# Kernel tuning notes

Hardware: AMD Instinct MI355X
Metric: run time of the kernel (lower is better)

The kernel has to match this reference:

```python
import jax, jax.numpy as jnp
import numpy as np

TAU = 0.1  # temperature (registered buffer, non-trainable)
EPS = 1e-12  # F.normalize eps


def setup_inputs() -> dict:
    key = jax.random.key(0)
    k1, k2 = jax.random.split(key)
    B, C = 4096, 512
    z1 = jax.random.normal(k1, (B, C), dtype=jnp.float32)
    z2 = jax.random.normal(k2, (B, C), dtype=jnp.float32)
    return {"z1": z1, "z2": z2}


def _l2_normalize(x):
    # matches F.normalize(p=2, dim=1): x / max(||x||, eps)
    n = jnp.sqrt(jnp.sum(x * x, axis=1, keepdims=True))
    return x / jnp.maximum(n, EPS)


def reference(z1, z2):
    B = z1.shape[0]
    N = 2 * B
    z = jnp.concatenate([_l2_normalize(z1), _l2_normalize(z2)], axis=0)  # [2B, C]
    # cosine similarity of unit vectors == dot product -> single GEMM
    S = jnp.exp((z @ z.T) / TAU)  # [2B, 2B]
    rows = jnp.arange(N)
    pos_cols = (rows + B) % N  # mask[r, c]=1 iff r == (c+B) mod 2B  <=> c == (r+B) mod 2B
    positive = S[rows, pos_cols]                 # [2B]
    # negatives = row sum over ~mask; note the original INCLUDES the diagonal
    negative = jnp.sum(S, axis=1) - positive     # [2B]
    pairs_loss = -jnp.log(positive / negative)   # [2B]
    loss = pairs_loss.reshape(2, B).sum(axis=0) / N  # [B]
    return loss.mean()  # reduce=True
```

## Files before the change

kernel.cpp:

```cpp
#include <hip/hip_runtime.h>
#include <hip/hip_bf16.h>


#define BDIM 4096
#define CDIM 512
#define NROWS 8192

typedef __attribute__((ext_vector_type(4))) float f32x4;
typedef __attribute__((ext_vector_type(8))) short bf16x8;

__device__ __forceinline__ unsigned short f2bf_rne(float x) {
    unsigned u = __float_as_uint(x);
    u += 0x7fffu + ((u >> 16) & 1u);
    return (unsigned short)(u >> 16);
}

__global__ __launch_bounds__(256) void normalize_kernel(
    const float* __restrict__ z1, const float* __restrict__ z2,
    unsigned short* __restrict__ zb, float* __restrict__ pos10) {
    const int w = threadIdx.x >> 6, lane = threadIdx.x & 63;
    const int r = blockIdx.x * 4 + w;
    const float4* p1 = (const float4*)(z1 + (size_t)r * CDIM);
    const float4* p2 = (const float4*)(z2 + (size_t)r * CDIM);
    float4 a0 = p1[lane], a1 = p1[64 + lane];
    float4 b0 = p2[lane], b1 = p2[64 + lane];
    float s1 = a0.x * a0.x + a0.y * a0.y + a0.z * a0.z + a0.w * a0.w +
               a1.x * a1.x + a1.y * a1.y + a1.z * a1.z + a1.w * a1.w;
    float s2 = b0.x * b0.x + b0.y * b0.y + b0.z * b0.z + b0.w * b0.w +
               b1.x * b1.x + b1.y * b1.y + b1.z * b1.z + b1.w * b1.w;
    float d = a0.x * b0.x + a0.y * b0.y + a0.z * b0.z + a0.w * b0.w +
              a1.x * b1.x + a1.y * b1.y + a1.z * b1.z + a1.w * b1.w;
#pragma unroll
    for (int m = 1; m < 64; m <<= 1) {
        s1 += __shfl_xor(s1, m, 64);
        s2 += __shfl_xor(s2, m, 64);
        d += __shfl_xor(d, m, 64);
    }
    const float n1 = fmaxf(sqrtf(s1), 1e-12f);
    const float n2 = fmaxf(sqrtf(s2), 1e-12f);
    const float i1 = 1.0f / n1, i2 = 1.0f / n2;
    ushort4 o;
    ushort4* q1 = (ushort4*)(zb + (size_t)r * CDIM);
    ushort4* q2 = (ushort4*)(zb + (size_t)(r + BDIM) * CDIM);
    o.x = f2bf_rne(a0.x * i1); o.y = f2bf_rne(a0.y * i1);
    o.z = f2bf_rne(a0.z * i1); o.w = f2bf_rne(a0.w * i1);
    q1[lane] = o;
    o.x = f2bf_rne(a1.x * i1); o.y = f2bf_rne(a1.y * i1);
    o.z = f2bf_rne(a1.z * i1); o.w = f2bf_rne(a1.w * i1);
    q1[64 + lane] = o;
    o.x = f2bf_rne(b0.x * i2); o.y = f2bf_rne(b0.y * i2);
    o.z = f2bf_rne(b0.z * i2); o.w = f2bf_rne(b0.w * i2);
    q2[lane] = o;
    o.x = f2bf_rne(b1.x * i2); o.y = f2bf_rne(b1.y * i2);
    o.z = f2bf_rne(b1.z * i2); o.w = f2bf_rne(b1.w * i2);
    q2[64 + lane] = o;
    if (lane == 0) pos10[r] = (d / (n1 * n2)) * 10.0f;
}

__global__ __launch_bounds__(256) void simgemm_kernel(
    const unsigned short* __restrict__ Z, float* __restrict__ rowsum) {
    const int bx = blockIdx.x, by = blockIdx.y;
    if (bx < by) return;
    const bool diag = (bx == by);

    __shared__ unsigned short Alds[128 * 64];
    __shared__ unsigned short Blds[128 * 64];

    const int t = threadIdx.x;
    const int lane = t & 63, w = t >> 6;
    const int wr = w >> 1, wc = w & 1;

    f32x4 acc[4][4] = {};

    const int srow = t >> 3;
    const int scolb = (((t & 7) ^ ((t >> 3) & 7)) << 4);
    const char* Zb = (const char*)Z;

    for (int k0 = 0; k0 < CDIM; k0 += 64) {
#pragma unroll
        for (int i = 0; i < 4; ++i) {
            const char* ga = Zb + ((size_t)(by * 128 + i * 32 + srow) << 10) + (k0 << 1) + scolb;
            __builtin_amdgcn_global_load_lds(
                (const __attribute__((address_space(1))) void*)ga,
                (__attribute__((address_space(3))) void*)(Alds + i * 2048 + w * 512),
                16, 0, 0);
        }
#pragma unroll
        for (int i = 0; i < 4; ++i) {
            const char* gb = Zb + ((size_t)(bx * 128 + i * 32 + srow) << 10) + (k0 << 1) + scolb;
            __builtin_amdgcn_global_load_lds(
                (const __attribute__((address_space(1))) void*)gb,
                (__attribute__((address_space(3))) void*)(Blds + i * 2048 + w * 512),
                16, 0, 0);
        }
        __syncthreads();

        const int sw = (lane & 7) << 4;
#pragma unroll
        for (int kk = 0; kk < 2; ++kk) {
            const int koff = (((lane >> 4) << 4) + kk * 64) ^ sw;
            bf16x8 af[4], bfr[4];
#pragma unroll
            for (int mi = 0; mi < 4; ++mi) {
                const int row = wr * 64 + mi * 16 + (lane & 15);
                af[mi] = *(const bf16x8*)((const char*)Alds + row * 128 + koff);
            }
#pragma unroll
            for (int ni = 0; ni < 4; ++ni) {
                const int row = wc * 64 + ni * 16 + (lane & 15);
                bfr[ni] = *(const bf16x8*)((const char*)Blds + row * 128 + koff);
            }
#pragma unroll
            for (int mi = 0; mi < 4; ++mi)
#pragma unroll
                for (int ni = 0; ni < 4; ++ni)
                    acc[mi][ni] = __builtin_amdgcn_mfma_f32_16x16x32_bf16(
                        af[mi], bfr[ni], acc[mi][ni], 0, 0, 0);
        }
        __syncthreads();
    }

    const float SC = 14.4269504088896340736f;
    const int g = lane >> 4;
    float cs[4] = {0.f, 0.f, 0.f, 0.f};
#pragma unroll
    for (int mi = 0; mi < 4; ++mi) {
        float rs0 = 0.f, rs1 = 0.f, rs2 = 0.f, rs3 = 0.f;
#pragma unroll
        for (int ni = 0; ni < 4; ++ni) {
            f32x4 a = acc[mi][ni];
            const float e0 = exp2f(a[0] * SC);
            const float e1 = exp2f(a[1] * SC);
            const float e2 = exp2f(a[2] * SC);
            const float e3 = exp2f(a[3] * SC);
            rs0 += e0; rs1 += e1; rs2 += e2; rs3 += e3;
            cs[ni] += (e0 + e1) + (e2 + e3);
        }
#pragma unroll
        for (int m = 1; m < 16; m <<= 1) {
            rs0 += __shfl_xor(rs0, m, 64);
            rs1 += __shfl_xor(rs1, m, 64);
            rs2 += __shfl_xor(rs2, m, 64);
            rs3 += __shfl_xor(rs3, m, 64);
        }
        if ((lane & 15) == 0) {
            const int rbase = by * 128 + wr * 64 + mi * 16 + g * 4;
            atomicAdd(&rowsum[rbase + 0], rs0);
            atomicAdd(&rowsum[rbase + 1], rs1);
            atomicAdd(&rowsum[rbase + 2], rs2);
            atomicAdd(&rowsum[rbase + 3], rs3);
        }
    }
    if (!diag) {
#pragma unroll
        for (int ni = 0; ni < 4; ++ni) {
            float c = cs[ni];
            c += __shfl_xor(c, 16, 64);
            c += __shfl_xor(c, 32, 64);
            if (lane < 16)
                atomicAdd(&rowsum[bx * 128 + wc * 64 + ni * 16 + lane], c);
        }
    }
}

__global__ __launch_bounds__(256) void finalize_kernel(
    const float* __restrict__ rowsum, const float* __restrict__ pos10,
    float* __restrict__ out) {
    __shared__ float sm[4];
    const int w = threadIdx.x >> 6, lane = threadIdx.x & 63;
    const int r = blockIdx.x * 256 + threadIdx.x;
    const float p10 = pos10[r];
    const float pos = expf(p10);
    float l = (logf(rowsum[r] - pos) - p10) +
              (logf(rowsum[r + BDIM] - pos) - p10);
#pragma unroll
    for (int m = 1; m < 64; m <<= 1) l += __shfl_xor(l, m, 64);
    if (lane == 0) sm[w] = l;
    __syncthreads();
    if (threadIdx.x == 0) {
        const float tot = sm[0] + sm[1] + sm[2] + sm[3];
        atomicAdd(out, tot * (1.0f / ((float)NROWS * (float)BDIM)));
    }
}

extern "C" void kernel_launch(void* const* d_in, const int* in_sizes, int n_in,
                              void* d_out, int out_size, void* d_ws, size_t ws_size,
                              hipStream_t stream) {
    const float* z1 = (const float*)d_in[0];
    const float* z2 = (const float*)d_in[1];
    float* out = (float*)d_out;
    unsigned short* zb = (unsigned short*)d_ws;
    float* rowsum = (float*)((char*)d_ws + (size_t)NROWS * CDIM * 2);
    float* pos10 = rowsum + NROWS;

    hipMemsetAsync(rowsum, 0, NROWS * sizeof(float), stream);
    hipMemsetAsync(out, 0, sizeof(float), stream);

    normalize_kernel<<<BDIM / 4, 256, 0, stream>>>(z1, z2, zb, pos10);
    dim3 g2(64, 64);
    simgemm_kernel<<<g2, 256, 0, stream>>>(zb, rowsum);
    finalize_kernel<<<BDIM / 256, 256, 0, stream>>>(rowsum, pos10, out);
}
```

Before: 162.4 us.

## Pack triangular GEMM tiles into persistent blocks with double-buffered LDS and fused finalize

Replaces the 64x64 grid with early-exiting lower-triangle blocks by a compact 544-block launch. Each block walks up to four consecutive column tiles of the upper triangle, reusing the A panel, with XCD-aware block remapping. The K loop is double-buffered in LDS so global-to-LDS loads for the next K slice (or the next tile) overlap the MFMA work. The memsets and the separate finalize kernel are removed: normalize zeroes the accumulators, and the last simgemm block, found by an atomic ticket, computes the loss. This doubles LDS use and adds a serial tail on one block.

```diff
diff --git a/kernel.cpp b/kernel.cpp
--- a/kernel.cpp
+++ b/kernel.cpp
@@ -5,9 +5,14 @@
 #define BDIM 4096
 #define CDIM 512
 #define NROWS 8192
+#define NTILE 64
+#define NBLK 544
 
 typedef __attribute__((ext_vector_type(4))) float f32x4;
 typedef __attribute__((ext_vector_type(8))) short bf16x8;
+
+#define AS1 __attribute__((address_space(1)))
+#define AS3 __attribute__((address_space(3)))
 
 __device__ __forceinline__ unsigned short f2bf_rne(float x) {
     unsigned u = __float_as_uint(x);
@@ -17,7 +22,14 @@
 
 __global__ __launch_bounds__(256) void normalize_kernel(
     const float* __restrict__ z1, const float* __restrict__ z2,
-    unsigned short* __restrict__ zb, float* __restrict__ pos10) {
+    unsigned short* __restrict__ zb, float* __restrict__ pos10,
+    float* __restrict__ rowsum, float* __restrict__ out,
+    unsigned* __restrict__ ticket) {
+    if (blockIdx.x == 0) {
+#pragma unroll
+        for (int i = 0; i < NROWS / 256; ++i) rowsum[i * 256 + threadIdx.x] = 0.f;
+        if (threadIdx.x == 0) { out[0] = 0.f; ticket[0] = 0u; }
+    }
     const int w = threadIdx.x >> 6, lane = threadIdx.x & 63;
     const int r = blockIdx.x * 4 + w;
     const float4* p1 = (const float4*)(z1 + (size_t)r * CDIM);
@@ -58,13 +70,23 @@
 }
 
 __global__ __launch_bounds__(256) void simgemm_kernel(
-    const unsigned short* __restrict__ Z, float* __restrict__ rowsum) {
-    const int bx = blockIdx.x, by = blockIdx.y;
-    if (bx < by) return;
-    const bool diag = (bx == by);
-
-    __shared__ unsigned short Alds[128 * 64];
-    __shared__ unsigned short Blds[128 * 64];
+    const unsigned short* __restrict__ Z, float* __restrict__ rowsum,
+    const float* __restrict__ pos10, float* __restrict__ out,
+    unsigned* __restrict__ ticket) {
+    const int orig = blockIdx.x;
+    int b = (orig & 7) * (NBLK / 8) + (orig >> 3);
+    int by = 0;
+    while (true) {
+        const int ch = (NTILE - by + 3) >> 2;
+        if (b < ch) break;
+        b -= ch; ++by;
+    }
+    const int bx0 = by + (b << 2);
+    const int NT = min(4, NTILE - bx0);
+
+    __shared__ unsigned short lds[2][2][128 * 64];
+    __shared__ float redsm[4];
+    __shared__ unsigned lastsm;
 
     const int t = threadIdx.x;
     const int lane = t & 63, w = t >> 6;
@@ -75,111 +97,132 @@
     const int srow = t >> 3;
     const int scolb = (((t & 7) ^ ((t >> 3) & 7)) << 4);
     const char* Zb = (const char*)Z;
-
-    for (int k0 = 0; k0 < CDIM; k0 += 64) {
-#pragma unroll
-        for (int i = 0; i < 4; ++i) {
-            const char* ga = Zb + ((size_t)(by * 128 + i * 32 + srow) << 10) + (k0 << 1) + scolb;
-            __builtin_amdgcn_global_load_lds(
-                (const __attribute__((address_space(1))) void*)ga,
-                (__attribute__((address_space(3))) void*)(Alds + i * 2048 + w * 512),
-                16, 0, 0);
-        }
-#pragma unroll
-        for (int i = 0; i < 4; ++i) {
-            const char* gb = Zb + ((size_t)(bx * 128 + i * 32 + srow) << 10) + (k0 << 1) + scolb;
-            __builtin_amdgcn_global_load_lds(
-                (const __attribute__((address_space(1))) void*)gb,
-                (__attribute__((address_space(3))) void*)(Blds + i * 2048 + w * 512),
-                16, 0, 0);
-        }
-        __syncthreads();
-
-        const int sw = (lane & 7) << 4;
-#pragma unroll
-        for (int kk = 0; kk < 2; ++kk) {
-            const int koff = (((lane >> 4) << 4) + kk * 64) ^ sw;
-            bf16x8 af[4], bfr[4];
-#pragma unroll
-            for (int mi = 0; mi < 4; ++mi) {
-                const int row = wr * 64 + mi * 16 + (lane & 15);
-                af[mi] = *(const bf16x8*)((const char*)Alds + row * 128 + koff);
-            }
-#pragma unroll
-            for (int ni = 0; ni < 4; ++ni) {
-                const int row = wc * 64 + ni * 16 + (lane & 15);
-                bfr[ni] = *(const bf16x8*)((const char*)Blds + row * 128 + koff);
-            }
-#pragma unroll
-            for (int mi = 0; mi < 4; ++mi)
-#pragma unroll
-                for (int ni = 0; ni < 4; ++ni)
-                    acc[mi][ni] = __builtin_amdgcn_mfma_f32_16x16x32_bf16(
-                        af[mi], bfr[ni], acc[mi][ni], 0, 0, 0);
-        }
-        __syncthreads();
+    const size_t apan = ((size_t)(by * 128) << 10);
+
+#define STG(kn, bpanv, db)                                                        \
+    {                                                                             \
+        const int kb_ = ((kn) << 7) + scolb;                                      \
+        _Pragma("unroll") for (int i_ = 0; i_ < 4; ++i_) {                        \
+            const size_t ro_ = ((size_t)(i_ * 32 + srow) << 10) + kb_;            \
+            __builtin_amdgcn_global_load_lds(                                     \
+                (const AS1 void*)(Zb + apan + ro_),                               \
+                (AS3 void*)((char*)&lds[db][0][0] + i_ * 4096 + w * 1024),        \
+                16, 0, 0);                                                        \
+            __builtin_amdgcn_global_load_lds(                                     \
+                (const AS1 void*)(Zb + (bpanv) + ro_),                            \
+                (AS3 void*)((char*)&lds[db][1][0] + i_ * 4096 + w * 1024),        \
+                16, 0, 0);                                                        \
+        }                                                                         \
     }
 
     const float SC = 14.4269504088896340736f;
     const int g = lane >> 4;
-    float cs[4] = {0.f, 0.f, 0.f, 0.f};
-#pragma unroll
-    for (int mi = 0; mi < 4; ++mi) {
-        float rs0 = 0.f, rs1 = 0.f, rs2 = 0.f, rs3 = 0.f;
-#pragma unroll
-        for (int ni = 0; ni < 4; ++ni) {
-            f32x4 a = acc[mi][ni];
-            const float e0 = exp2f(a[0] * SC);
-            const float e1 = exp2f(a[1] * SC);
-            const float e2 = exp2f(a[2] * SC);
-            const float e3 = exp2f(a[3] * SC);
-            rs0 += e0; rs1 += e1; rs2 += e2; rs3 += e3;
-            cs[ni] += (e0 + e1) + (e2 + e3);
-        }
-#pragma unroll
-        for (int m = 1; m < 16; m <<= 1) {
-            rs0 += __shfl_xor(rs0, m, 64);
-            rs1 += __shfl_xor(rs1, m, 64);
-            rs2 += __shfl_xor(rs2, m, 64);
-            rs3 += __shfl_xor(rs3, m, 64);
-        }
-        if ((lane & 15) == 0) {
-            const int rbase = by * 128 + wr * 64 + mi * 16 + g * 4;
-            atomicAdd(&rowsum[rbase + 0], rs0);
-            atomicAdd(&rowsum[rbase + 1], rs1);
-            atomicAdd(&rowsum[rbase + 2], rs2);
-            atomicAdd(&rowsum[rbase + 3], rs3);
-        }
-    }
-    if (!diag) {
-#pragma unroll
-        for (int ni = 0; ni < 4; ++ni) {
-            float c = cs[ni];
-            c += __shfl_xor(c, 16, 64);
-            c += __shfl_xor(c, 32, 64);
-            if (lane < 16)
-                atomicAdd(&rowsum[bx * 128 + wc * 64 + ni * 16 + lane], c);
-        }
-    }
-}
-
-__global__ __launch_bounds__(256) void finalize_kernel(
-    const float* __restrict__ rowsum, const float* __restrict__ pos10,
-    float* __restrict__ out) {
-    __shared__ float sm[4];
-    const int w = threadIdx.x >> 6, lane = threadIdx.x & 63;
-    const int r = blockIdx.x * 256 + threadIdx.x;
-    const float p10 = pos10[r];
-    const float pos = expf(p10);
-    float l = (logf(rowsum[r] - pos) - p10) +
-              (logf(rowsum[r + BDIM] - pos) - p10);
-#pragma unroll
-    for (int m = 1; m < 64; m <<= 1) l += __shfl_xor(l, m, 64);
-    if (lane == 0) sm[w] = l;
+    const int swz = (lane & 7) << 4;
+
+    STG(0, ((size_t)(bx0 * 128) << 10), 0);
     __syncthreads();
-    if (threadIdx.x == 0) {
-        const float tot = sm[0] + sm[1] + sm[2] + sm[3];
-        atomicAdd(out, tot * (1.0f / ((float)NROWS * (float)BDIM)));
+
+    for (int jt = 0; jt < NT; ++jt) {
+        const int bx = bx0 + jt;
+        const size_t bpan_n = ((size_t)((bx + 1) * 128) << 10);
+#pragma unroll
+        for (int k = 0; k < 8; ++k) {
+            const int cur = k & 1;
+            if (k < 7) {
+                STG(k + 1, ((size_t)(bx * 128) << 10), cur ^ 1);
+            } else if (jt + 1 < NT) {
+                STG(0, bpan_n, cur ^ 1);
+            }
+            const char* Ab = (const char*)&lds[cur][0][0];
+            const char* Bb = (const char*)&lds[cur][1][0];
+#pragma unroll
+            for (int kk = 0; kk < 2; ++kk) {
+                const int koff = (((lane >> 4) << 4) + kk * 64) ^ swz;
+                bf16x8 af[4], bfr[4];
+#pragma unroll
+                for (int mi = 0; mi < 4; ++mi) {
+                    const int row = wr * 64 + mi * 16 + (lane & 15);
+                    af[mi] = *(const bf16x8*)(Ab + row * 128 + koff);
+                }
+#pragma unroll
+                for (int ni = 0; ni < 4; ++ni) {
+                    const int row = wc * 64 + ni * 16 + (lane & 15);
+                    bfr[ni] = *(const bf16x8*)(Bb + row * 128 + koff);
+                }
+#pragma unroll
+                for (int mi = 0; mi < 4; ++mi)
+#pragma unroll
+                    for (int ni = 0; ni < 4; ++ni)
+                        acc[mi][ni] = __builtin_amdgcn_mfma_f32_16x16x32_bf16(
+                            af[mi], bfr[ni], acc[mi][ni], 0, 0, 0);
+            }
+            __syncthreads();
+        }
+
+        const bool diag = (bx == by);
+        float cs[4] = {0.f, 0.f, 0.f, 0.f};
+#pragma unroll
+        for (int mi = 0; mi < 4; ++mi) {
+            float rs0 = 0.f, rs1 = 0.f, rs2 = 0.f, rs3 = 0.f;
+#pragma unroll
+            for (int ni = 0; ni < 4; ++ni) {
+                f32x4 a = acc[mi][ni];
+                const float e0 = exp2f(a[0] * SC);
+                const float e1 = exp2f(a[1] * SC);
+                const float e2 = exp2f(a[2] * SC);
+                const float e3 = exp2f(a[3] * SC);
+                rs0 += e0; rs1 += e1; rs2 += e2; rs3 += e3;
+                cs[ni] += (e0 + e1) + (e2 + e3);
+                acc[mi][ni][0] = 0.f; acc[mi][ni][1] = 0.f;
+                acc[mi][ni][2] = 0.f; acc[mi][ni][3] = 0.f;
+            }
+#pragma unroll
+            for (int m = 1; m < 16; m <<= 1) {
+                rs0 += __shfl_xor(rs0, m, 64);
+                rs1 += __shfl_xor(rs1, m, 64);
+                rs2 += __shfl_xor(rs2, m, 64);
+                rs3 += __shfl_xor(rs3, m, 64);
+            }
+            if ((lane & 15) == 0) {
+                const int rbase = by * 128 + wr * 64 + mi * 16 + g * 4;
+                atomicAdd(&rowsum[rbase + 0], rs0);
+                atomicAdd(&rowsum[rbase + 1], rs1);
+                atomicAdd(&rowsum[rbase + 2], rs2);
+                atomicAdd(&rowsum[rbase + 3], rs3);
+            }
+        }
+        if (!diag) {
+#pragma unroll
+            for (int ni = 0; ni < 4; ++ni) {
+                float c = cs[ni];
+                c += __shfl_xor(c, 16, 64);
+                c += __shfl_xor(c, 32, 64);
+                if (lane < 16)
+                    atomicAdd(&rowsum[bx * 128 + wc * 64 + ni * 16 + lane], c);
+            }
+        }
+    }
+#undef STG
+
+    __threadfence();
+    if (t == 0) lastsm = (atomicAdd(ticket, 1u) == (unsigned)(NBLK - 1)) ? 1u : 0u;
+    __syncthreads();
+    if (lastsm) {
+        float l = 0.f;
+        for (int r = t; r < BDIM; r += 256) {
+            const float rs1 = atomicAdd(&rowsum[r], 0.f);
+            const float rs2 = atomicAdd(&rowsum[r + BDIM], 0.f);
+            const float p10 = pos10[r];
+            const float pos = expf(p10);
+            l += (logf(rs1 - pos) - p10) + (logf(rs2 - pos) - p10);
+        }
+#pragma unroll
+        for (int m = 1; m < 64; m <<= 1) l += __shfl_xor(l, m, 64);
+        if (lane == 0) redsm[w] = l;
+        __syncthreads();
+        if (t == 0)
+            out[0] = (redsm[0] + redsm[1] + redsm[2] + redsm[3]) *
+                     (1.0f / ((float)NROWS * (float)BDIM));
     }
 }
 
@@ -192,12 +235,8 @@
     unsigned short* zb = (unsigned short*)d_ws;
     float* rowsum = (float*)((char*)d_ws + (size_t)NROWS * CDIM * 2);
     float* pos10 = rowsum + NROWS;
-
-    hipMemsetAsync(rowsum, 0, NROWS * sizeof(float), stream);
-    hipMemsetAsync(out, 0, sizeof(float), stream);
-
-    normalize_kernel<<<BDIM / 4, 256, 0, stream>>>(z1, z2, zb, pos10);
-    dim3 g2(64, 64);
-    simgemm_kernel<<<g2, 256, 0, stream>>>(zb, rowsum);
-    finalize_kernel<<<BDIM / 256, 256, 0, stream>>>(rowsum, pos10, out);
-}
+    unsigned* ticket = (unsigned*)(pos10 + BDIM);
+
+    normalize_kernel<<<BDIM / 4, 256, 0, stream>>>(z1, z2, zb, pos10, rowsum, out, ticket);
+    simgemm_kernel<<<NBLK, 256, 0, stream>>>(zb, rowsum, pos10, out, ticket);
+}
```

Measured after the change: 224.6 us. 1.38x slower.
